# Optimization experiments

Hardware: AMD Instinct MI355X
Metric: run time of the kernel (lower is better)

The kernel has to match this reference:

```python
import jax, jax.numpy as jnp
import numpy as np

B, N, DN = 8, 4096, 64
E = 1048576
H, DM = 128, 64   # message MLP: 2*DN -> H -> DM
HU, F = 128, 64   # node-update MLP: DN+DM -> HU -> F


def setup_inputs() -> dict:
    key = jax.random.key(0)
    ks = jax.random.split(key, 13)
    inp = {
        'node_feats': jax.random.normal(ks[0], (B, N, DN), dtype=jnp.float32),
        'edge_b': jax.random.randint(ks[1], (E,), 0, B, dtype=jnp.int32),
        'edge_src': jax.random.randint(ks[2], (E,), 0, N, dtype=jnp.int32),
        'edge_dst': jax.random.randint(ks[3], (E,), 0, N, dtype=jnp.int32),
        'edge_vals': jax.random.uniform(ks[4], (E,), dtype=jnp.float32),
        # message MLP params (Dense-relu, Dense-linear)
        'Wm1': jax.random.normal(ks[5], (2 * DN, H), dtype=jnp.float32) / np.sqrt(2 * DN),
        'bm1': jnp.zeros((H,), jnp.float32),
        'Wm2': jax.random.normal(ks[6], (H, DM), dtype=jnp.float32) / np.sqrt(H),
        'bm2': jnp.zeros((DM,), jnp.float32),
        # node-update MLP params
        'Wu1': jax.random.normal(ks[7], (DN + DM, HU), dtype=jnp.float32) / np.sqrt(DN + DM),
        'bu1': jnp.zeros((HU,), jnp.float32),
        'Wu2': jax.random.normal(ks[8], (HU, F), dtype=jnp.float32) / np.sqrt(HU),
        'bu2': jnp.zeros((F,), jnp.float32),
    }
    return inp


def reference(node_feats, edge_b, edge_src, edge_dst, edge_vals,
              Wm1, bm1, Wm2, bm2, Wu1, bu1, Wu2, bu2):
    # --- create messages: gather src/target feats per edge ---
    src_feats = node_feats[edge_b, edge_src]            # (E, DN)
    tgt_feats = node_feats[edge_b, edge_dst]            # (E, DN)
    feats = jnp.concatenate([src_feats, tgt_feats], axis=-1)  # (E, 2*DN)
    h = jax.nn.relu(feats @ Wm1 + bm1)
    messages = h @ Wm2 + bm2                            # (E, DM)

    # --- gather (scatter) messages: weighted ragged segment-mean ---
    weighted = messages * edge_vals[:, None]            # (E, DM)
    seg = edge_b * N + edge_src                          # rowids b*max_N + src
    sums = jax.ops.segment_sum(weighted, seg, num_segments=B * N)
    counts = jax.ops.segment_sum(jnp.ones((E,), weighted.dtype), seg,
                                 num_segments=B * N)
    gathered = sums / jnp.maximum(counts, 1.0)[:, None]  # mean; 0 for empty rows
    gathered = gathered.reshape(B, N, DM)

    # --- update nodes ---
    upd_in = jnp.concatenate([node_feats, gathered], axis=-1)  # (B, N, DN+DM)
    hu = jax.nn.relu(upd_in @ Wu1 + bu1)
    updated = hu @ Wu2 + bu2                            # (B, N, F)
    return updated
```

## Files before the change

kernel.cpp:

```cpp
#include <hip/hip_runtime.h>

#define NB 8
#define NN 4096
#define DNF 64
#define NEDGE 1048576
#define DM 64
#define FF 64

#define NBKT2 2048
#define SPB2 16
#define REGCAP 768
#define OVFCAP 65536

using f32x4 = __attribute__((ext_vector_type(4))) float;
using s16x8 = __attribute__((ext_vector_type(8))) short;

__device__ __forceinline__ unsigned short f2b(float f) {
    union { float f; unsigned u; } v; v.f = f;
    unsigned r = (v.u + 0x7fffu + ((v.u >> 16) & 1u)) >> 16;
    return (unsigned short)r;
}
__device__ __forceinline__ float uif(unsigned u) {
    union { unsigned u; float f; } v; v.u = u;
    return v.f;
}

__device__ __forceinline__ void pack_one(const float* __restrict__ W,
                                         unsigned short* __restrict__ out,
                                         int K, int Ncols, int idx) {
    int j = idx & 7;
    int lane = (idx >> 3) & 63;
    int frag = idx >> 9;
    int KS = K >> 5;
    int ks = frag % KS;
    int nt = frag / KS;
    int k = ks * 32 + ((lane >> 4) << 3) + j;
    int col = nt * 16 + (lane & 15);
    out[idx] = f2b(W[k * Ncols + col]);
}

__global__ void pack_all(const float* __restrict__ Wm1, const float* __restrict__ Wm2,
                         const float* __restrict__ Wu1, const float* __restrict__ Wu2,
                         unsigned short* __restrict__ Qw, unsigned short* __restrict__ Pw,
                         unsigned short* __restrict__ Wm2p,
                         unsigned short* __restrict__ Wu1p, unsigned short* __restrict__ Wu2p) {
    int idx = blockIdx.x * 256 + threadIdx.x;
    if (idx < 8192)        pack_one(Wm1,              Qw,   64, 128, idx);
    else if (idx < 16384)  pack_one(Wm1 + 64 * 128,   Pw,   64, 128, idx - 8192);
    else if (idx < 24576)  pack_one(Wm2,              Wm2p, 128, 64, idx - 16384);
    else if (idx < 40960)  pack_one(Wu1,              Wu1p, 128, 128, idx - 24576);
    else                   pack_one(Wu2,              Wu2p, 128, 64, idx - 40960);
}

__global__ void pack_weights(const float* __restrict__ W, unsigned short* __restrict__ out,
                             int K, int Ncols) {
    int idx = blockIdx.x * 256 + threadIdx.x;
    if (idx >= K * Ncols) return;
    pack_one(W, out, K, Ncols, idx);
}

__launch_bounds__(256, 4)
__global__ void precompute_pq(const float* __restrict__ X,
                              const unsigned short* __restrict__ Qw,
                              const unsigned short* __restrict__ Pw,
                              const float* __restrict__ b1,
                              unsigned short* __restrict__ Qp,
                              unsigned short* __restrict__ Pp) {
    __shared__ unsigned short A[64][72];
    const int tid = threadIdx.x;
    const int g0 = blockIdx.x * 64;
    for (int i = 0; i < 16; ++i) {
        int idx = i * 256 + tid;
        int node = idx >> 6;
        int f = idx & 63;
        A[node][f] = f2b(X[(size_t)(g0 + node) * DNF + f]);
    }
    __syncthreads();
    const int wave = tid >> 6, lane = tid & 63;
    const int lr = lane & 15, lq = lane >> 4;
    const int arow = wave * 16 + lr;
    s16x8 a[2];
#pragma unroll
    for (int ks = 0; ks < 2; ++ks)
        a[ks] = *reinterpret_cast<const s16x8*>(&A[arow][ks * 32 + lq * 8]);
#pragma unroll
    for (int nt = 0; nt < 8; ++nt) {
        f32x4 accQ = {0.f, 0.f, 0.f, 0.f};
        f32x4 accP = {0.f, 0.f, 0.f, 0.f};
#pragma unroll
        for (int ks = 0; ks < 2; ++ks) {
            s16x8 bq = *reinterpret_cast<const s16x8*>(&Qw[(((nt << 1) + ks) * 64 + lane) * 8]);
            s16x8 bp = *reinterpret_cast<const s16x8*>(&Pw[(((nt << 1) + ks) * 64 + lane) * 8]);
            accQ = __builtin_amdgcn_mfma_f32_16x16x32_bf16(a[ks], bq, accQ, 0, 0, 0);
            accP = __builtin_amdgcn_mfma_f32_16x16x32_bf16(a[ks], bp, accP, 0, 0, 0);
        }
        int col = nt * 16 + lr;
        float bias = b1[col];
#pragma unroll
        for (int j = 0; j < 4; ++j) {
            int row = g0 + wave * 16 + lq * 4 + j;
            Qp[(size_t)row * 128 + col] = f2b(accQ[j] + bias);
            Pp[(size_t)row * 128 + col] = f2b(accP[j]);
        }
    }
}

__launch_bounds__(256, 8)
__global__ void scatter16(const int* __restrict__ eb, const int* __restrict__ esrc,
                          const int* __restrict__ edst, const float* __restrict__ evals,
                          unsigned* __restrict__ gcur, unsigned* __restrict__ payslot,
                          unsigned* __restrict__ ovf_cnt, unsigned* __restrict__ ovf_seg,
                          unsigned* __restrict__ ovf_pay) {
    const int t0 = blockIdx.x * 512 + threadIdx.x;
#pragma unroll
    for (int k = 0; k < 2; ++k) {
        int e = t0 + k * 256;
        int seg = eb[e] * NN + esrc[e];
        unsigned wq = (unsigned)fminf(evals[e] * 8192.0f + 0.5f, 8191.0f);
        unsigned pay = (unsigned)edst[e] | (wq << 12) | ((unsigned)(seg & 15) << 25);
        int bkt = seg >> 4;
        unsigned pos = atomicAdd(&gcur[bkt * 32], 1u);
        if (pos < (unsigned)REGCAP) {
            payslot[(size_t)bkt * REGCAP + pos] = pay;
        } else {
            unsigned o = atomicAdd(ovf_cnt, 1u);
            if (o < (unsigned)OVFCAP) { ovf_seg[o] = (unsigned)seg; ovf_pay[o] = pay; }
        }
    }
}

__launch_bounds__(256, 6)
__global__ void bucket16_fused(const unsigned short* __restrict__ Qp,
                               const unsigned short* __restrict__ Pp,
                               const unsigned* __restrict__ payslot,
                               const unsigned* __restrict__ gcur,
                               const unsigned* __restrict__ ovf_cnt,
                               const unsigned* __restrict__ ovf_seg,
                               const unsigned* __restrict__ ovf_pay,
                               const unsigned short* __restrict__ Wm2p,
                               const float* __restrict__ b2m,
                               const float* __restrict__ X,
                               const unsigned short* __restrict__ Wu1p,
                               const float* __restrict__ bu1,
                               const unsigned short* __restrict__ Wu2p,
                               const float* __restrict__ bu2,
                               float* __restrict__ out) {
    __shared__ unsigned sorted[REGCAP];
    __shared__ unsigned short S[16][136];
    __shared__ unsigned short A1[16][136];
    __shared__ unsigned short Hs[16][136];
    __shared__ unsigned h[16];
    __shared__ unsigned offs[17];
    __shared__ unsigned curb[16];
    __shared__ float SW[16], SC[16];
    const int tid = threadIdx.x, wv = tid >> 6, lane = tid & 63;
    const int bkt = blockIdx.x;
    const int node0 = bkt * SPB2;
    const int rowbase = (bkt >> 8) << 12;
    const unsigned cnt = min(gcur[bkt * 32], (unsigned)REGCAP);
    const unsigned novf = ovf_cnt[0];

#pragma unroll
    for (int i = 0; i < 4; ++i) {
        int idx = i * 256 + tid;
        int row = idx >> 6, f = idx & 63;
        A1[row][f] = f2b(X[(size_t)(node0 + row) * DNF + f]);
    }
    if (tid < 16) h[tid] = 0;
    __syncthreads();
    for (unsigned i = tid; i < cnt; i += 256) {
        unsigned v = payslot[(size_t)bkt * REGCAP + i];
        atomicAdd(&h[(v >> 25) & 15u], 1u);
    }
    __syncthreads();
    if (tid < 16) {
        int x = (int)h[tid];
#pragma unroll
        for (int o = 1; o < 16; o <<= 1) {
            int y = __shfl_up(x, o);
            if (tid >= o) x += y;
        }
        offs[tid + 1] = (unsigned)x;
        if (tid == 0) offs[0] = 0;
    }
    __syncthreads();
    if (tid < 16) curb[tid] = offs[tid];
    __syncthreads();
    for (unsigned i = tid; i < cnt; i += 256) {
        unsigned v = payslot[(size_t)bkt * REGCAP + i];
        unsigned pos = atomicAdd(&curb[(v >> 25) & 15u], 1u);
        sorted[pos] = v;
    }
    __syncthreads();

    const unsigned* P32 = reinterpret_cast<const unsigned*>(Pp);
    const unsigned* Q32 = reinterpret_cast<const unsigned*>(Qp);
    for (int si = 0; si < 4; ++si) {
        const int lo = wv * 4 + si;
        const int seg = node0 + lo;
        const unsigned s0 = offs[lo], s1 = offs[lo + 1];
        unsigned qv = Q32[(size_t)seg * 64 + lane];
        float q0 = uif(qv << 16);
        float q1 = uif(qv & 0xffff0000u);
        float acc0 = 0.f, acc1 = 0.f, wsum = 0.f;
        unsigned scnt = s1 - s0;

        for (unsigned bse = s0; bse < s1; bse += 8) {
            unsigned pv[8]; float wf[8];
#pragma unroll
            for (int k = 0; k < 8; ++k) {
                unsigned idx = bse + (unsigned)k;
                unsigned c = (idx < s1) ? sorted[idx] : 0u;
                wf[k] = (float)((c >> 12) & 8191u) * (1.0f / 8192.0f);
                pv[k] = P32[(size_t)(rowbase + (int)(c & 0xfffu)) * 64 + lane];
            }
#pragma unroll
            for (int k = 0; k < 8; ++k) {
                float p0 = uif(pv[k] << 16);
                float p1 = uif(pv[k] & 0xffff0000u);
                acc0 = fmaf(wf[k], fmaxf(q0 + p0, 0.f), acc0);
                acc1 = fmaf(wf[k], fmaxf(q1 + p1, 0.f), acc1);
                wsum += wf[k];
            }
        }
        if (novf > 0) {
            unsigned ncl = min(novf, (unsigned)OVFCAP);
            for (unsigned i = 0; i < ncl; ++i) {
                if (ovf_seg[i] == (unsigned)seg) {
                    unsigned c = ovf_pay[i];
                    float w = (float)((c >> 12) & 8191u) * (1.0f / 8192.0f);
                    unsigned pv = P32[(size_t)(rowbase + (int)(c & 0xfffu)) * 64 + lane];
                    acc0 = fmaf(w, fmaxf(q0 + uif(pv << 16), 0.f), acc0);
                    acc1 = fmaf(w, fmaxf(q1 + uif(pv & 0xffff0000u), 0.f), acc1);
                    wsum += w;
                    scnt += 1;
                }
            }
        }
        unsigned sp = (unsigned)f2b(acc0) | ((unsigned)f2b(acc1) << 16);
        *reinterpret_cast<unsigned*>(&S[lo][2 * lane]) = sp;
        if (lane == 0) {
            SW[lo] = wsum;
            SC[lo] = 1.0f / (float)max(scnt, 1u);
        }
    }
    __syncthreads();

    const int lr = lane & 15, lq = lane >> 4;
    {
        s16x8 a[4];
#pragma unroll
        for (int ks = 0; ks < 4; ++ks)
            a[ks] = *reinterpret_cast<const s16x8*>(&S[lr][ks * 32 + lq * 8]);
        f32x4 acc = {0.f, 0.f, 0.f, 0.f};
#pragma unroll
        for (int ks = 0; ks < 4; ++ks) {
            s16x8 bf = *reinterpret_cast<const s16x8*>(&Wm2p[(((wv << 2) + ks) * 64 + lane) * 8]);
            acc = __builtin_amdgcn_mfma_f32_16x16x32_bf16(a[ks], bf, acc, 0, 0, 0);
        }
        float bb = b2m[wv * 16 + lr];
#pragma unroll
        for (int j = 0; j < 4; ++j) {
            int r = lq * 4 + j;
            float g = (acc[j] + SW[r] * bb) * SC[r];
            A1[r][64 + wv * 16 + lr] = f2b(g);
        }
    }
    __syncthreads();

    {
        s16x8 a1[4];
#pragma unroll
        for (int ks = 0; ks < 4; ++ks)
            a1[ks] = *reinterpret_cast<const s16x8*>(&A1[lr][ks * 32 + lq * 8]);
#pragma unroll
        for (int t = 0; t < 2; ++t) {
            int nt = wv * 2 + t;
            f32x4 acc = {0.f, 0.f, 0.f, 0.f};
#pragma unroll
            for (int ks = 0; ks < 4; ++ks) {
                s16x8 bf = *reinterpret_cast<const s16x8*>(&Wu1p[(((nt << 2) + ks) * 64 + lane) * 8]);
                acc = __builtin_amdgcn_mfma_f32_16x16x32_bf16(a1[ks], bf, acc, 0, 0, 0);
            }
            float bias = bu1[nt * 16 + lr];
#pragma unroll
            for (int j = 0; j < 4; ++j) {
                float hh = fmaxf(acc[j] + bias, 0.f);
                Hs[lq * 4 + j][nt * 16 + lr] = f2b(hh);
            }
        }
    }
    __syncthreads();

    {
        s16x8 a2[4];
#pragma unroll
        for (int ks = 0; ks < 4; ++ks)
            a2[ks] = *reinterpret_cast<const s16x8*>(&Hs[lr][ks * 32 + lq * 8]);
        f32x4 acc = {0.f, 0.f, 0.f, 0.f};
#pragma unroll
        for (int ks = 0; ks < 4; ++ks) {
            s16x8 bf = *reinterpret_cast<const s16x8*>(&Wu2p[(((wv << 2) + ks) * 64 + lane) * 8]);
            acc = __builtin_amdgcn_mfma_f32_16x16x32_bf16(a2[ks], bf, acc, 0, 0, 0);
        }
        float bias = bu2[wv * 16 + lr];
#pragma unroll
        for (int j = 0; j < 4; ++j)
            out[(size_t)(node0 + lq * 4 + j) * FF + wv * 16 + lr] = acc[j] + bias;
    }
}


template<int SCALE>
__launch_bounds__(256, 4)
__global__ void node_kernel(const float* __restrict__ node_feats,
                            const float* __restrict__ sums, const float* __restrict__ counts,
                            const unsigned short* __restrict__ W1p, const float* __restrict__ b1,
                            const unsigned short* __restrict__ W2p, const float* __restrict__ b2,
                            float* __restrict__ out) {
    __shared__ unsigned short A1[64][136];
    __shared__ unsigned short Hs[64][136];
    const int tid = threadIdx.x;
    const int g0 = blockIdx.x * 64;
    for (int i = 0; i < 16; ++i) {
        int idx = i * 256 + tid;
        int node = idx >> 6;
        int p = idx & 63;
        int g = g0 + node;
        float2 v;
        if (p < 32) {
            v = *reinterpret_cast<const float2*>(node_feats + (size_t)g * DNF + 2 * p);
        } else {
            float2 s = *reinterpret_cast<const float2*>(sums + (size_t)g * DM + 2 * p - 64);
            if (SCALE) {
                float scale = 1.0f / fmaxf(counts[g], 1.0f);
                s.x *= scale; s.y *= scale;
            }
            v = s;
        }
        unsigned packed = (unsigned)f2b(v.x) | ((unsigned)f2b(v.y) << 16);
        *reinterpret_cast<unsigned*>(&A1[node][2 * p]) = packed;
    }
    __syncthreads();
    const int wave = tid >> 6, lane = tid & 63;
    const int lr = lane & 15, lq = lane >> 4;
    const int arow = wave * 16 + lr;
    s16x8 a[4];
#pragma unroll
    for (int ks = 0; ks < 4; ++ks)
        a[ks] = *reinterpret_cast<const s16x8*>(&A1[arow][ks * 32 + lq * 8]);
#pragma unroll
    for (int nt = 0; nt < 8; ++nt) {
        f32x4 acc = {0.f, 0.f, 0.f, 0.f};
#pragma unroll
        for (int ks = 0; ks < 4; ++ks) {
            s16x8 bf = *reinterpret_cast<const s16x8*>(&W1p[(((nt << 2) + ks) * 64 + lane) * 8]);
            acc = __builtin_amdgcn_mfma_f32_16x16x32_bf16(a[ks], bf, acc, 0, 0, 0);
        }
        float bias = b1[nt * 16 + lr];
#pragma unroll
        for (int j = 0; j < 4; ++j) {
            float h = acc[j] + bias;
            h = h > 0.f ? h : 0.f;
            Hs[wave * 16 + lq * 4 + j][nt * 16 + lr] = f2b(h);
        }
    }
    s16x8 a2[4];
#pragma unroll
    for (int ks = 0; ks < 4; ++ks)
        a2[ks] = *reinterpret_cast<const s16x8*>(&Hs[arow][ks * 32 + lq * 8]);
#pragma unroll
    for (int nt = 0; nt < 4; ++nt) {
        f32x4 acc = {0.f, 0.f, 0.f, 0.f};
#pragma unroll
        for (int ks = 0; ks < 4; ++ks) {
            s16x8 bf = *reinterpret_cast<const s16x8*>(&W2p[(((nt << 2) + ks) * 64 + lane) * 8]);
            acc = __builtin_amdgcn_mfma_f32_16x16x32_bf16(a2[ks], bf, acc, 0, 0, 0);
        }
        float bias = b2[nt * 16 + lr];
#pragma unroll
        for (int j = 0; j < 4; ++j) {
            int g = g0 + wave * 16 + lq * 4 + j;
            out[(size_t)g * FF + nt * 16 + lr] = acc[j] + bias;
        }
    }
}

__launch_bounds__(256, 4)
__global__ void edge_kernel(const float* __restrict__ node_feats,
                            const int* __restrict__ eb, const int* __restrict__ esrc,
                            const int* __restrict__ edst, const float* __restrict__ evals,
                            const unsigned short* __restrict__ W1p, const float* __restrict__ b1,
                            const unsigned short* __restrict__ W2p, const float* __restrict__ b2,
                            float* __restrict__ sums, float* __restrict__ counts) {
    __shared__ unsigned short A1[64][136];
    __shared__ unsigned short Hs[64][136];
    const int tid = threadIdx.x;
    const int e0 = blockIdx.x * 64;
    if (tid < 64) {
        int e = e0 + tid;
        atomicAdd(&counts[eb[e] * NN + esrc[e]], 1.0f);
    }
    for (int i = 0; i < 16; ++i) {
        int idx = i * 256 + tid;
        int edge = idx >> 6;
        int p = idx & 63;
        int e = e0 + edge;
        int b = eb[e];
        const float* row;
        if (p < 32) row = node_feats + ((size_t)b * NN + esrc[e]) * DNF;
        else        row = node_feats + ((size_t)b * NN + edst[e]) * DNF - 64;
        float2 v = *reinterpret_cast<const float2*>(row + 2 * p);
        unsigned packed = (unsigned)f2b(v.x) | ((unsigned)f2b(v.y) << 16);
        *reinterpret_cast<unsigned*>(&A1[edge][2 * p]) = packed;
    }
    __syncthreads();
    const int wave = tid >> 6, lane = tid & 63;
    const int lr = lane & 15, lq = lane >> 4;
    const int arow = wave * 16 + lr;
    s16x8 a[4];
#pragma unroll
    for (int ks = 0; ks < 4; ++ks)
        a[ks] = *reinterpret_cast<const s16x8*>(&A1[arow][ks * 32 + lq * 8]);
#pragma unroll
    for (int nt = 0; nt < 8; ++nt) {
        f32x4 acc = {0.f, 0.f, 0.f, 0.f};
#pragma unroll
        for (int ks = 0; ks < 4; ++ks) {
            s16x8 bf = *reinterpret_cast<const s16x8*>(&W1p[(((nt << 2) + ks) * 64 + lane) * 8]);
            acc = __builtin_amdgcn_mfma_f32_16x16x32_bf16(a[ks], bf, acc, 0, 0, 0);
        }
        float bias = b1[nt * 16 + lr];
#pragma unroll
        for (int j = 0; j < 4; ++j) {
            float h = acc[j] + bias;
            h = h > 0.f ? h : 0.f;
            Hs[wave * 16 + lq * 4 + j][nt * 16 + lr] = f2b(h);
        }
    }
    s16x8 a2[4];
#pragma unroll
    for (int ks = 0; ks < 4; ++ks)
        a2[ks] = *reinterpret_cast<const s16x8*>(&Hs[arow][ks * 32 + lq * 8]);
    float ev[4]; int seg4[4];
#pragma unroll
    for (int j = 0; j < 4; ++j) {
        int r = e0 + wave * 16 + lq * 4 + j;
        ev[j] = evals[r];
        seg4[j] = eb[r] * NN + esrc[r];
    }
#pragma unroll
    for (int nt = 0; nt < 4; ++nt) {
        f32x4 acc = {0.f, 0.f, 0.f, 0.f};
#pragma unroll
        for (int ks = 0; ks < 4; ++ks) {
            s16x8 bf = *reinterpret_cast<const s16x8*>(&W2p[(((nt << 2) + ks) * 64 + lane) * 8]);
            acc = __builtin_amdgcn_mfma_f32_16x16x32_bf16(a2[ks], bf, acc, 0, 0, 0);
        }
        float bias = b2[nt * 16 + lr];
#pragma unroll
        for (int j = 0; j < 4; ++j) {
            float m = (acc[j] + bias) * ev[j];
            atomicAdd(&sums[(size_t)seg4[j] * DM + nt * 16 + lr], m);
        }
    }
}

extern "C" void kernel_launch(void* const* d_in, const int* in_sizes, int n_in,
                              void* d_out, int out_size, void* d_ws, size_t ws_size,
                              hipStream_t stream) {
    const float* node_feats = (const float*)d_in[0];
    const int*   eb    = (const int*)d_in[1];
    const int*   esrc  = (const int*)d_in[2];
    const int*   edst  = (const int*)d_in[3];
    const float* evals = (const float*)d_in[4];
    const float* Wm1 = (const float*)d_in[5];
    const float* bm1 = (const float*)d_in[6];
    const float* Wm2 = (const float*)d_in[7];
    const float* bm2 = (const float*)d_in[8];
    const float* Wu1 = (const float*)d_in[9];
    const float* bu1 = (const float*)d_in[10];
    const float* Wu2 = (const float*)d_in[11];
    const float* bu2 = (const float*)d_in[12];
    float* out = (float*)d_out;
    char* ws = (char*)d_ws;

    const size_t NEED = 23953536;
    if (ws_size >= NEED) {
        unsigned short* Qp      = (unsigned short*)(ws);
        unsigned short* Pp      = (unsigned short*)(ws + 8388608);
        unsigned*       payslot = (unsigned*)(ws + 16777216);
        unsigned*       gcur    = (unsigned*)(ws + 23068672);
        unsigned*       ovf_cnt = (unsigned*)(ws + 23330816);
        unsigned*       ovf_seg = (unsigned*)(ws + 23330944);
        unsigned*       ovf_pay = (unsigned*)(ws + 23593088);
        unsigned short* Qw      = (unsigned short*)(ws + 23855232);
        unsigned short* Pw      = (unsigned short*)(ws + 23871616);
        unsigned short* Wu1p    = (unsigned short*)(ws + 23888000);
        unsigned short* Wu2p    = (unsigned short*)(ws + 23920768);
        unsigned short* Wm2p    = (unsigned short*)(ws + 23937152);

        hipMemsetAsync(gcur, 0, 262144 + 128, stream);
        pack_all<<<192, 256, 0, stream>>>(Wm1, Wm2, Wu1, Wu2, Qw, Pw, Wm2p, Wu1p, Wu2p);
        precompute_pq<<<512, 256, 0, stream>>>(node_feats, Qw, Pw, bm1, Qp, Pp);
        scatter16<<<NEDGE / 512, 256, 0, stream>>>(eb, esrc, edst, evals,
                                                   gcur, payslot, ovf_cnt, ovf_seg, ovf_pay);
        bucket16_fused<<<NBKT2, 256, 0, stream>>>(Qp, Pp, payslot, gcur,
                                                  ovf_cnt, ovf_seg, ovf_pay,
                                                  Wm2p, bm2, node_feats,
                                                  Wu1p, bu1, Wu2p, bu2, out);
    } else {
        float* counts          = (float*)ws;
        unsigned short* W1p    = (unsigned short*)(ws + 131072);
        unsigned short* W2p    = (unsigned short*)(ws + 163840);
        unsigned short* Wu1p   = (unsigned short*)(ws + 180224);
        unsigned short* Wu2p   = (unsigned short*)(ws + 212992);
        hipMemsetAsync(d_out, 0, (size_t)out_size * sizeof(float), stream);
        hipMemsetAsync(counts, 0, 32768 * sizeof(float), stream);
        pack_weights<<<64, 256, 0, stream>>>(Wm1, W1p, 128, 128);
        pack_weights<<<32, 256, 0, stream>>>(Wm2, W2p, 128, 64);
        pack_weights<<<64, 256, 0, stream>>>(Wu1, Wu1p, 128, 128);
        pack_weights<<<32, 256, 0, stream>>>(Wu2, Wu2p, 128, 64);
        edge_kernel<<<NEDGE / 64, 256, 0, stream>>>(node_feats, eb, esrc, edst, evals,
                                                    W1p, bm1, W2p, bm2, out, counts);
        node_kernel<1><<<(NB * NN) / 64, 256, 0, stream>>>(node_feats, out, counts,
                                                           Wu1p, bu1, Wu2p, bu2, out);
    }
}
```

Before: 120.2 us.

## Split edge bucket counters per XCD to localize scatter atomics

The scatter kernel now reads the hardware XCC id and keeps a separate counter and payload sub-slot per XCD for each bucket, so atomics from different chiplets never hit the same cache line. It also handles 4 edges per thread and issues all their atomics before the stores. The fused bucket kernel merges the 8 sub-slots when building its histogram and sorted list. This raises workspace use and lowers per-sub-slot capacity to 192, which may push more edges onto the global overflow path if buckets are skewed. It also drops the old 32-word padding between counters.

```diff
diff --git a/kernel.cpp b/kernel.cpp
--- a/kernel.cpp
+++ b/kernel.cpp
@@ -9,7 +9,8 @@
 
 #define NBKT2 2048
 #define SPB2 16
-#define REGCAP 768
+#define NXCD 8
+#define SUBCAP 192
 #define OVFCAP 65536
 
 using f32x4 = __attribute__((ext_vector_type(4))) float;
@@ -106,25 +107,34 @@
 }
 
 __launch_bounds__(256, 8)
-__global__ void scatter16(const int* __restrict__ eb, const int* __restrict__ esrc,
-                          const int* __restrict__ edst, const float* __restrict__ evals,
-                          unsigned* __restrict__ gcur, unsigned* __restrict__ payslot,
-                          unsigned* __restrict__ ovf_cnt, unsigned* __restrict__ ovf_seg,
-                          unsigned* __restrict__ ovf_pay) {
-    const int t0 = blockIdx.x * 512 + threadIdx.x;
-#pragma unroll
-    for (int k = 0; k < 2; ++k) {
+__global__ void scatter_xcd(const int* __restrict__ eb, const int* __restrict__ esrc,
+                            const int* __restrict__ edst, const float* __restrict__ evals,
+                            unsigned* __restrict__ gcurX, unsigned* __restrict__ payslot,
+                            unsigned* __restrict__ ovf_cnt, unsigned* __restrict__ ovf_seg,
+                            unsigned* __restrict__ ovf_pay) {
+    unsigned xcd;
+    asm volatile("s_getreg_b32 %0, hwreg(HW_REG_XCC_ID)" : "=s"(xcd));
+    xcd &= (NXCD - 1);
+    const int t0 = blockIdx.x * 1024 + threadIdx.x;
+    int seg[4]; unsigned pk[4];
+#pragma unroll
+    for (int k = 0; k < 4; ++k) {
         int e = t0 + k * 256;
-        int seg = eb[e] * NN + esrc[e];
+        seg[k] = eb[e] * NN + esrc[e];
         unsigned wq = (unsigned)fminf(evals[e] * 8192.0f + 0.5f, 8191.0f);
-        unsigned pay = (unsigned)edst[e] | (wq << 12) | ((unsigned)(seg & 15) << 25);
-        int bkt = seg >> 4;
-        unsigned pos = atomicAdd(&gcur[bkt * 32], 1u);
-        if (pos < (unsigned)REGCAP) {
-            payslot[(size_t)bkt * REGCAP + pos] = pay;
+        pk[k] = (unsigned)edst[e] | (wq << 12) | ((unsigned)(seg[k] & 15) << 25);
+    }
+    unsigned pos[4];
+#pragma unroll
+    for (int k = 0; k < 4; ++k)
+        pos[k] = atomicAdd(&gcurX[xcd * NBKT2 + (seg[k] >> 4)], 1u);
+#pragma unroll
+    for (int k = 0; k < 4; ++k) {
+        if (pos[k] < (unsigned)SUBCAP) {
+            payslot[((size_t)(seg[k] >> 4) * NXCD + xcd) * SUBCAP + pos[k]] = pk[k];
         } else {
             unsigned o = atomicAdd(ovf_cnt, 1u);
-            if (o < (unsigned)OVFCAP) { ovf_seg[o] = (unsigned)seg; ovf_pay[o] = pay; }
+            if (o < (unsigned)OVFCAP) { ovf_seg[o] = (unsigned)seg[k]; ovf_pay[o] = pk[k]; }
         }
     }
 }
@@ -133,7 +143,7 @@
 __global__ void bucket16_fused(const unsigned short* __restrict__ Qp,
                                const unsigned short* __restrict__ Pp,
                                const unsigned* __restrict__ payslot,
-                               const unsigned* __restrict__ gcur,
+                               const unsigned* __restrict__ gcurX,
                                const unsigned* __restrict__ ovf_cnt,
                                const unsigned* __restrict__ ovf_seg,
                                const unsigned* __restrict__ ovf_pay,
@@ -145,19 +155,19 @@
                                const unsigned short* __restrict__ Wu2p,
                                const float* __restrict__ bu2,
                                float* __restrict__ out) {
-    __shared__ unsigned sorted[REGCAP];
+    __shared__ unsigned sorted[NXCD * SUBCAP];
     __shared__ unsigned short S[16][136];
     __shared__ unsigned short A1[16][136];
     __shared__ unsigned short Hs[16][136];
     __shared__ unsigned h[16];
     __shared__ unsigned offs[17];
     __shared__ unsigned curb[16];
+    __shared__ unsigned cx[NXCD];
     __shared__ float SW[16], SC[16];
     const int tid = threadIdx.x, wv = tid >> 6, lane = tid & 63;
     const int bkt = blockIdx.x;
     const int node0 = bkt * SPB2;
     const int rowbase = (bkt >> 8) << 12;
-    const unsigned cnt = min(gcur[bkt * 32], (unsigned)REGCAP);
     const unsigned novf = ovf_cnt[0];
 
 #pragma unroll
@@ -167,29 +177,36 @@
         A1[row][f] = f2b(X[(size_t)(node0 + row) * DNF + f]);
     }
     if (tid < 16) h[tid] = 0;
-    __syncthreads();
-    for (unsigned i = tid; i < cnt; i += 256) {
-        unsigned v = payslot[(size_t)bkt * REGCAP + i];
-        atomicAdd(&h[(v >> 25) & 15u], 1u);
+    if (tid < NXCD) cx[tid] = min(gcurX[tid * NBKT2 + bkt], (unsigned)SUBCAP);
+    __syncthreads();
+    for (int x = 0; x < NXCD; ++x) {
+        unsigned c = cx[x];
+        for (unsigned i = tid; i < c; i += 256) {
+            unsigned v = payslot[((size_t)bkt * NXCD + x) * SUBCAP + i];
+            atomicAdd(&h[(v >> 25) & 15u], 1u);
+        }
     }
     __syncthreads();
     if (tid < 16) {
-        int x = (int)h[tid];
+        int xx = (int)h[tid];
 #pragma unroll
         for (int o = 1; o < 16; o <<= 1) {
-            int y = __shfl_up(x, o);
-            if (tid >= o) x += y;
-        }
-        offs[tid + 1] = (unsigned)x;
+            int y = __shfl_up(xx, o);
+            if (tid >= o) xx += y;
+        }
+        offs[tid + 1] = (unsigned)xx;
         if (tid == 0) offs[0] = 0;
     }
     __syncthreads();
     if (tid < 16) curb[tid] = offs[tid];
     __syncthreads();
-    for (unsigned i = tid; i < cnt; i += 256) {
-        unsigned v = payslot[(size_t)bkt * REGCAP + i];
-        unsigned pos = atomicAdd(&curb[(v >> 25) & 15u], 1u);
-        sorted[pos] = v;
+    for (int x = 0; x < NXCD; ++x) {
+        unsigned c = cx[x];
+        for (unsigned i = tid; i < c; i += 256) {
+            unsigned v = payslot[((size_t)bkt * NXCD + x) * SUBCAP + i];
+            unsigned pos = atomicAdd(&curb[(v >> 25) & 15u], 1u);
+            sorted[pos] = v;
+        }
     }
     __syncthreads();
 
@@ -485,27 +502,27 @@
     float* out = (float*)d_out;
     char* ws = (char*)d_ws;
 
-    const size_t NEED = 23953536;
+    const size_t NEED = 30048384;
     if (ws_size >= NEED) {
         unsigned short* Qp      = (unsigned short*)(ws);
         unsigned short* Pp      = (unsigned short*)(ws + 8388608);
         unsigned*       payslot = (unsigned*)(ws + 16777216);
-        unsigned*       gcur    = (unsigned*)(ws + 23068672);
-        unsigned*       ovf_cnt = (unsigned*)(ws + 23330816);
-        unsigned*       ovf_seg = (unsigned*)(ws + 23330944);
-        unsigned*       ovf_pay = (unsigned*)(ws + 23593088);
-        unsigned short* Qw      = (unsigned short*)(ws + 23855232);
-        unsigned short* Pw      = (unsigned short*)(ws + 23871616);
-        unsigned short* Wu1p    = (unsigned short*)(ws + 23888000);
-        unsigned short* Wu2p    = (unsigned short*)(ws + 23920768);
-        unsigned short* Wm2p    = (unsigned short*)(ws + 23937152);
-
-        hipMemsetAsync(gcur, 0, 262144 + 128, stream);
+        unsigned*       gcurX   = (unsigned*)(ws + 29360128);
+        unsigned*       ovf_cnt = (unsigned*)(ws + 29425664);
+        unsigned*       ovf_seg = (unsigned*)(ws + 29425792);
+        unsigned*       ovf_pay = (unsigned*)(ws + 29687936);
+        unsigned short* Qw      = (unsigned short*)(ws + 29950080);
+        unsigned short* Pw      = (unsigned short*)(ws + 29966464);
+        unsigned short* Wu1p    = (unsigned short*)(ws + 29982848);
+        unsigned short* Wu2p    = (unsigned short*)(ws + 30015616);
+        unsigned short* Wm2p    = (unsigned short*)(ws + 30032000);
+
+        hipMemsetAsync(gcurX, 0, 65536 + 128, stream);
         pack_all<<<192, 256, 0, stream>>>(Wm1, Wm2, Wu1, Wu2, Qw, Pw, Wm2p, Wu1p, Wu2p);
         precompute_pq<<<512, 256, 0, stream>>>(node_feats, Qw, Pw, bm1, Qp, Pp);
-        scatter16<<<NEDGE / 512, 256, 0, stream>>>(eb, esrc, edst, evals,
-                                                   gcur, payslot, ovf_cnt, ovf_seg, ovf_pay);
-        bucket16_fused<<<NBKT2, 256, 0, stream>>>(Qp, Pp, payslot, gcur,
+        scatter_xcd<<<NEDGE / 1024, 256, 0, stream>>>(eb, esrc, edst, evals,
+                                                      gcurX, payslot, ovf_cnt, ovf_seg, ovf_pay);
+        bucket16_fused<<<NBKT2, 256, 0, stream>>>(Qp, Pp, payslot, gcurX,
                                                   ovf_cnt, ovf_seg, ovf_pay,
                                                   Wm2p, bm2, node_feats,
                                                   Wu1p, bu1, Wu2p, bu2, out);
```

Result: faster. 114.6 us (-4.6%).
